# Performance work log

Measured on AMD Instinct MI355X. Metric: run time of the kernel, lower is better.

The kernel has to match this reference:

```python
import jax, jax.numpy as jnp
import numpy as np

B, S, H = 1, 2048, 1024
NH, NKV, D = 8, 2, 128           # query heads, kv heads, head_dim
E, TOPK = 64, 6                   # experts per modality, top-k
IT, IV, IS = 512, 256, 1024       # text / vision expert inter, shared inter (=512*2)
THETA = 500000.0
SECTIONS = (22, 22, 20)           # h, w, t rotary freq split; sum = D//2
EPS = 1e-5


def rmsnorm(x, w):
    return x * w * jax.lax.rsqrt(jnp.mean(x * x, axis=-1, keepdims=True) + EPS)


def apply_mrope(x, positions):
    # x: [B,S,h,D]; positions: [3,B,S] (h, w, t position streams)
    inv_freq = 1.0 / (THETA ** (jnp.arange(0, D, 2, dtype=jnp.float32) / D))  # [D//2]
    axis_idx = np.repeat(np.arange(3), SECTIONS)              # which pos stream per freq band
    pos = jnp.transpose(positions[axis_idx], (1, 2, 0)).astype(jnp.float32)  # [B,S,D//2]
    freqs = pos * inv_freq
    cos = jnp.cos(freqs)[:, :, None, :]
    sin = jnp.sin(freqs)[:, :, None, :]
    x1, x2 = x[..., 0::2], x[..., 1::2]                       # interleaved (non-neox)
    o1 = x1 * cos - x2 * sin
    o2 = x1 * sin + x2 * cos
    return jnp.stack([o1, o2], axis=-1).reshape(x.shape)


def attention(x, positions, w_qkv, w_o):
    b, s, _ = x.shape
    qkv = x @ w_qkv
    q, k, v = jnp.split(qkv, [NH * D, NH * D + NKV * D], axis=-1)
    q = q.reshape(b, s, NH, D)
    k = k.reshape(b, s, NKV, D)
    v = v.reshape(b, s, NKV, D)
    q = apply_mrope(q, positions)
    k = apply_mrope(k, positions)
    rep = NH // NKV
    k = jnp.repeat(k, rep, axis=2)
    v = jnp.repeat(v, rep, axis=2)
    scores = jnp.einsum('bqhd,bkhd->bhqk', q, k) * (D ** -0.5)
    causal = jnp.tril(jnp.ones((s, s), bool))
    scores = jnp.where(causal, scores, -jnp.inf)
    attn = jax.nn.softmax(scores, axis=-1)
    out = jnp.einsum('bhqk,bkhd->bqhd', attn, v).reshape(b, s, NH * D)
    return out @ w_o


def mlp(x, wg, wu, wd):
    return (jax.nn.silu(x @ wg) * (x @ wu)) @ wd


def moe_branch(x, gate_w, bias, wg, wu, wd):
    # x: [T,H]; gate_w: [H,E] fp32; bias: [E] fp32 correction bias
    logits = x.astype(jnp.float32) @ gate_w                   # [T,E]
    scores = jax.nn.sigmoid(logits)
    _, topi = jax.lax.top_k(scores + bias[None, :], TOPK)     # bias only picks experts
    w = jnp.take_along_axis(scores, topi, axis=-1)            # weights from raw scores
    w = w / jnp.sum(w, axis=-1, keepdims=True)                # renormalize
    T = x.shape[0]
    gates = jnp.zeros((T, E), jnp.float32).at[jnp.arange(T)[:, None], topi].set(w)
    g = jax.nn.silu(jnp.einsum('th,ehi->eti', x, wg)) * jnp.einsum('th,ehi->eti', x, wu)
    g = g * gates.T[:, :, None].astype(x.dtype)               # fold routing weights pre-down-proj
    return jnp.einsum('eti,eih->th', g, wd)


def _forward(hidden_states, positions, visual_token_mask, w_qkv, w_o, ln1_w, ln2_w,
             text_gate_w, vision_gate_w, corr_bias, tw_gate, tw_up, tw_down,
             vw_gate, vw_up, vw_down, sw_gate, sw_up, sw_down):
    h = hidden_states + attention(rmsnorm(hidden_states, ln1_w), positions, w_qkv, w_o)
    x = rmsnorm(h, ln2_w).reshape(-1, H)                      # [T,H]
    shared = mlp(x, sw_gate, sw_up, sw_down)
    text_out = moe_branch(x, text_gate_w, corr_bias[0], tw_gate, tw_up, tw_down)
    vision_out = moe_branch(x, vision_gate_w, corr_bias[1], vw_gate, vw_up, vw_down)
    mask = visual_token_mask.reshape(-1, 1)
    moe_out = jnp.where(mask, vision_out, text_out) + shared
    return h + moe_out.reshape(h.shape)


def setup_inputs() -> dict:
    key = jax.random.key(0)
    ks = jax.random.split(key, 16)
    rn = lambda i, shape, s: jax.random.normal(ks[i], shape, jnp.float32) * s
    return dict(
        hidden_states=rn(0, (B, S, H), 1.0),
        positions=jnp.broadcast_to(jnp.arange(S, dtype=jnp.int32)[None, None, :], (3, B, S)),
        visual_token_mask=jax.random.bernoulli(ks[1], 0.3, (B, S)),
        w_qkv=rn(2, (H, (NH + 2 * NKV) * D), H ** -0.5),
        w_o=rn(3, (NH * D, H), (NH * D) ** -0.5),
        ln1_w=jnp.ones((H,), jnp.float32),
        ln2_w=jnp.ones((H,), jnp.float32),
        text_gate_w=rn(4, (H, E), H ** -0.5),
        vision_gate_w=rn(5, (H, E), H ** -0.5),
        corr_bias=rn(6, (2, E), 0.02),
        tw_gate=rn(7, (E, H, IT), H ** -0.5),
        tw_up=rn(8, (E, H, IT), H ** -0.5),
        tw_down=rn(9, (E, IT, H), IT ** -0.5),
        vw_gate=rn(10, (E, H, IV), H ** -0.5),
        vw_up=rn(11, (E, H, IV), H ** -0.5),
        vw_down=rn(12, (E, IV, H), IV ** -0.5),
        sw_gate=rn(13, (H, IS), H ** -0.5),
        sw_up=rn(14, (H, IS), H ** -0.5),
        sw_down=rn(15, (IS, H), IS ** -0.5),
    )


def reference(hidden_states, positions, visual_token_mask, w_qkv, w_o, ln1_w, ln2_w,
              text_gate_w, vision_gate_w, corr_bias, tw_gate, tw_up, tw_down,
              vw_gate, vw_up, vw_down, sw_gate, sw_up, sw_down):
    return _forward(hidden_states, positions, visual_token_mask, w_qkv, w_o, ln1_w, ln2_w,
                    text_gate_w, vision_gate_w, corr_bias, tw_gate, tw_up, tw_down,
                    vw_gate, vw_up, vw_down, sw_gate, sw_up, sw_down)
```

## Files before the change

### kernel.cpp

```cpp
#include <hip/hip_runtime.h>
#include <hip/hip_bf16.h>
#include <math.h>

#define TT   2048
#define HID  1024
#define NHEAD 8
#define NKVH  2
#define HD   128
#define QKVN 1536
#define NEXP 64
#define NTOP 6
#define I_T  512
#define I_V  256
#define I_S  1024
#define SBASE ((size_t)12288 * 512)
#define NCHUNK 576

typedef unsigned short u16;
typedef __attribute__((ext_vector_type(8))) short short8v;
typedef __attribute__((ext_vector_type(4))) float f32x4;

__device__ inline u16 f2bf(float f) {
  __hip_bfloat16 h = __float2bfloat16(f);
  return *reinterpret_cast<u16*>(&h);
}
__device__ inline float bfu2f(u16 u) {
  unsigned x = ((unsigned)u) << 16;
  return __uint_as_float(x);
}
__device__ inline void split2(float f, u16& h, u16& l) {
  h = f2bf(f);
  l = f2bf(f - bfu2f(h));
}
__device__ inline void split8(const float* f, u16* h, u16* l) {
#pragma unroll
  for (int i = 0; i < 8; ++i) split2(f[i], h[i], l[i]);
}

__device__ inline f32x4 mfma16(short8v a, short8v b, f32x4 c) {
  return __builtin_amdgcn_mfma_f32_16x16x32_bf16(a, b, c, 0, 0, 0);
}

__device__ inline void wload(const float* __restrict__ W, int ldw, int c0, int kc,
                             float4* r) {
  const int t = threadIdx.x;
  const int c4 = (t & 7) << 2;
  const int r0 = t >> 3;
#pragma unroll
  for (int j = 0; j < 4; ++j)
    r[j] = *(const float4*)&W[(size_t)(kc + r0 + j * 32) * ldw + c0 + c4];
}
__device__ inline void wwrite(const float4* r, u16* lds) {
  const int t = threadIdx.x;
  const int c4 = (t & 7) << 2;
  const int r0 = t >> 3;
#pragma unroll
  for (int j = 0; j < 4; ++j) {
    int k = r0 + j * 32;
    u16* dst = lds + ((k >> 3) * 32) * 8 + (k & 7);
    dst[(c4 + 0) * 8] = f2bf(r[j].x);
    dst[(c4 + 1) * 8] = f2bf(r[j].y);
    dst[(c4 + 2) * 8] = f2bf(r[j].z);
    dst[(c4 + 3) * 8] = f2bf(r[j].w);
  }
}

template<bool F32, bool BF, bool LO>
__global__ __launch_bounds__(256) void rmsnorm_kernel(const float* __restrict__ x,
                                                      const float* __restrict__ w,
                                                      float* __restrict__ o32,
                                                      u16* __restrict__ obfH,
                                                      u16* __restrict__ obfL) {
  const int row = blockIdx.x;
  const int t = threadIdx.x;
  const float4 v = *(const float4*)(x + (size_t)row * HID + t * 4);
  float ss = v.x*v.x + v.y*v.y + v.z*v.z + v.w*v.w;
#pragma unroll
  for (int m = 32; m >= 1; m >>= 1) ss += __shfl_xor(ss, m);
  __shared__ float red[4];
  __shared__ float rrs;
  if ((t & 63) == 0) red[t >> 6] = ss;
  __syncthreads();
  if (t == 0) rrs = rsqrtf((red[0] + red[1] + red[2] + red[3]) * (1.0f / HID) + 1e-5f);
  __syncthreads();
  const float rr = rrs;
  const float4 wv = *(const float4*)(w + t * 4);
  float o[4];
  o[0] = v.x * wv.x * rr; o[1] = v.y * wv.y * rr;
  o[2] = v.z * wv.z * rr; o[3] = v.w * wv.w * rr;
  if (F32) *(float4*)(o32 + (size_t)row * HID + t * 4) = *(float4*)o;
  if (BF) {
    u16 h[4], l[4];
#pragma unroll
    for (int i = 0; i < 4; ++i) split2(o[i], h[i], l[i]);
    *(uint2*)(obfH + (size_t)row * HID + t * 4) = *(uint2*)h;
    if (LO) *(uint2*)(obfL + (size_t)row * HID + t * 4) = *(uint2*)l;
  }
}

__global__ __launch_bounds__(256) void convert_w(const float* __restrict__ W, int N,
                                                 u16* __restrict__ PH,
                                                 u16* __restrict__ PL) {
  const int c = blockIdx.x * 256 + threadIdx.x;
  const int k8 = blockIdx.y;
  float f[8];
#pragma unroll
  for (int e = 0; e < 8; ++e) f[e] = W[(size_t)(k8 * 8 + e) * N + c];
  u16 h8[8], l8[8];
  split8(f, h8, l8);
  size_t gi = ((size_t)(c >> 5) * 128 + k8) * 256 + (size_t)(c & 31) * 8;
  *(uint4*)&PH[gi] = *(uint4*)h8;
  *(uint4*)&PL[gi] = *(uint4*)l8;
}

template<bool RES>
__global__ __launch_bounds__(256) void dense_split(const u16* __restrict__ AH,
                                                   const u16* __restrict__ AL,
                                                   const u16* __restrict__ WPH,
                                                   const u16* __restrict__ WPL,
                                                   const float* __restrict__ resid,
                                                   float* __restrict__ C, int N) {
  __shared__ u16 sWH[32768], sWL[32768];
  __shared__ u16 sAH[4096],  sAL[4096];
  const int t = threadIdx.x;
  const int cs = blockIdx.x;
  const int c0 = cs * 32;
  const int rows = TT / gridDim.y;
  const int mstart = blockIdx.y * rows, mend = mstart + rows;
  {
    const u16* gh = WPH + (size_t)cs * 32768;
    const u16* gl = WPL + (size_t)cs * 32768;
#pragma unroll
    for (int r = 0; r < 16; ++r) {
      int i8 = (t + 256 * r) * 8;
      *(uint4*)&sWH[i8] = *(const uint4*)&gh[i8];
      *(uint4*)&sWL[i8] = *(const uint4*)&gl[i8];
    }
  }
  const int w = t >> 6, lane = t & 63;
  const int rowHalf = (w & 1) << 4, colHalf = (w >> 1) << 4;
  for (int m0 = mstart; m0 < mend; m0 += 32) {
    f32x4 hh = {0.f,0.f,0.f,0.f}, hl = {0.f,0.f,0.f,0.f};
    f32x4 lh = {0.f,0.f,0.f,0.f}, ll = {0.f,0.f,0.f,0.f};
    for (int kc = 0; kc < HID; kc += 128) {
      __syncthreads();
#pragma unroll
      for (int r = 0; r < 2; ++r) {
        int task = t + 256 * r;
        int row = task >> 4, kg = task & 15;
        size_t g = (size_t)(m0 + row) * HID + kc + kg * 8;
        *(uint4*)&sAH[(kg * 32 + row) * 8] = *(const uint4*)&AH[g];
        *(uint4*)&sAL[(kg * 32 + row) * 8] = *(const uint4*)&AL[g];
      }
      __syncthreads();
#pragma unroll
      for (int ks = 0; ks < 4; ++ks) {
        int arow = rowHalf + (lane & 15);
        int akg = ks * 4 + (lane >> 4);
        short8v ah = *(const short8v*)&sAH[(akg * 32 + arow) * 8];
        short8v al = *(const short8v*)&sAL[(akg * 32 + arow) * 8];
        int wcol = colHalf + (lane & 15);
        int wkg = (kc >> 3) + ks * 4 + (lane >> 4);
        short8v bh = *(const short8v*)&sWH[(wkg * 32 + wcol) * 8];
        short8v bl = *(const short8v*)&sWL[(wkg * 32 + wcol) * 8];
        hh = mfma16(ah, bh, hh);
        hl = mfma16(ah, bl, hl);
        lh = mfma16(al, bh, lh);
        ll = mfma16(al, bl, ll);
      }
    }
    f32x4 acc = (hh + hl) + (lh + ll);
#pragma unroll
    for (int i = 0; i < 4; ++i) {
      int r = m0 + rowHalf + ((lane >> 4) << 2) + i;
      int c = c0 + colHalf + (lane & 15);
      float v = acc[i];
      if (RES) v += resid[(size_t)r * N + c];
      C[(size_t)r * N + c] = v;
    }
  }
}

__global__ __launch_bounds__(256) void pack_qkv(const float* __restrict__ qkv,
                                                const int* __restrict__ pos,
                                                u16* __restrict__ Qh, u16* __restrict__ Ql,
                                                u16* __restrict__ Kph, u16* __restrict__ Kpl,
                                                u16* __restrict__ Vph, u16* __restrict__ Vpl) {
  const int tile = blockIdx.x;
  const int t = threadIdx.x;
  __shared__ float cs[2048], sn[2048];
  for (int i = t; i < 2048; i += 256) {
    int tok32 = i >> 6, fi = i & 63;
    int tok = tile * 32 + tok32;
    int axis = (fi < 22) ? 0 : (fi < 44 ? 1 : 2);
    float posv = (float)pos[axis * TT + tok];
    float invf = powf(500000.0f, -((float)(2 * fi)) / 128.0f);
    float ang = posv * invf;
    sincosf(ang, &sn[i], &cs[i]);
  }
  __syncthreads();
  for (int task = t; task < 4096; task += 256) {
    int h = task >> 9;
    int rem = task & 511;
    int tok32 = rem >> 4, fi4 = rem & 15;
    int tok = tile * 32 + tok32;
    const float* src = qkv + (size_t)tok * QKVN + h * HD + fi4 * 8;
    float4 v0 = *(const float4*)src, v1 = *(const float4*)(src + 4);
    float f[8] = {v0.x, v0.y, v0.z, v0.w, v1.x, v1.y, v1.z, v1.w};
    float o[8];
#pragma unroll
    for (int j = 0; j < 4; ++j) {
      int fi = fi4 * 4 + j;
      float c = cs[tok32 * 64 + fi], s = sn[tok32 * 64 + fi];
      o[2*j]   = f[2*j] * c - f[2*j+1] * s;
      o[2*j+1] = f[2*j] * s + f[2*j+1] * c;
    }
    u16 h8[8], l8[8];
    split8(o, h8, l8);
    size_t d = (size_t)tok * HID + h * HD + fi4 * 8;
    *(uint4*)&Qh[d] = *(uint4*)h8;
    *(uint4*)&Ql[d] = *(uint4*)l8;
  }
  for (int task = t; task < 1024; task += 256) {
    int kvh = task >> 9;
    int rem = task & 511;
    int kk = rem >> 4, fi4 = rem & 15;
    int tok = tile * 32 + kk;
    const float* src = qkv + (size_t)tok * QKVN + NHEAD * HD + kvh * HD + fi4 * 8;
    float4 v0 = *(const float4*)src, v1 = *(const float4*)(src + 4);
    float f[8] = {v0.x, v0.y, v0.z, v0.w, v1.x, v1.y, v1.z, v1.w};
    float o[8];
#pragma unroll
    for (int j = 0; j < 4; ++j) {
      int fi = fi4 * 4 + j;
      float c = cs[kk * 64 + fi], s = sn[kk * 64 + fi];
      o[2*j]   = f[2*j] * c - f[2*j+1] * s;
      o[2*j+1] = f[2*j] * s + f[2*j+1] * c;
    }
    u16 h8[8], l8[8];
    split8(o, h8, l8);
    size_t d = ((size_t)(kvh * 64 + tile) << 12) + (size_t)(fi4 * 32 + kk) * 8;
    *(uint4*)&Kph[d] = *(uint4*)h8;
    *(uint4*)&Kpl[d] = *(uint4*)l8;
  }
  for (int task = t; task < 1024; task += 256) {
    int kvh = task >> 9;
    int rem = task & 511;
    int g = rem >> 7, dcol = rem & 127;
    float f[8];
#pragma unroll
    for (int e = 0; e < 8; ++e)
      f[e] = qkv[(size_t)(tile * 32 + g * 8 + e) * QKVN + (NHEAD + NKVH) * HD + kvh * HD + dcol];
    u16 h8[8], l8[8];
    split8(f, h8, l8);
    size_t d = ((size_t)(kvh * 64 + tile) << 12) + (size_t)(g * 128 + dcol) * 8;
    *(uint4*)&Vph[d] = *(uint4*)h8;
    *(uint4*)&Vpl[d] = *(uint4*)l8;
  }
}

__global__ void chunk_setup(int* __restrict__ tab, int* __restrict__ startOff) {
  if (threadIdx.x == 0 && blockIdx.x == 0) {
    int idx = 0;
    for (int qb = 0; qb < TT / 16; ++qb) {
      startOff[qb] = idx;
      int nkt = (qb >> 1) + 1;
      int nch = (nkt + 7) >> 3;
      for (int c = 0; c < nch; ++c) { tab[idx] = qb * 16 + c; ++idx; }
    }
  }
}

__global__ __launch_bounds__(256) void attn_part(const u16* __restrict__ Qh,
                                                 const u16* __restrict__ Ql,
                                                 const u16* __restrict__ Kph,
                                                 const u16* __restrict__ Kpl,
                                                 const u16* __restrict__ Vph,
                                                 const u16* __restrict__ Vpl,
                                                 const int* __restrict__ tab,
                                                 float* __restrict__ Opart,
                                                 float* __restrict__ Mpart,
                                                 float* __restrict__ Lpart) {
  const int ci = blockIdx.x;
  const int kvh = blockIdx.y;
  const int w = threadIdx.x >> 6, lane = threadIdx.x & 63;
  const int head = kvh * 4 + w;
  const int ent = tab[ci];
  const int qb = ent >> 4, cc = ent & 15;
  const int qw0 = qb * 16;
  const int lrow = lane & 15, loct = lane >> 4;
  const int nkt = (qb >> 1) + 1;
  const int kt0 = cc * 8, kt1 = min(kt0 + 8, nkt);

  __shared__ u16 Ph[4][512], Pl[4][512];

  short8v qh[4], ql[4];
  {
    const size_t qoff = (size_t)(qw0 + lrow) * HID + head * HD + loct * 8;
#pragma unroll
    for (int dc = 0; dc < 4; ++dc) {
      qh[dc] = *(const short8v*)&Qh[qoff + dc * 32];
      ql[dc] = *(const short8v*)&Ql[qoff + dc * 32];
    }
  }

  f32x4 o[8];
#pragma unroll
  for (int dt = 0; dt < 8; ++dt) o[dt] = (f32x4){0.f,0.f,0.f,0.f};
  float mr[4] = {-INFINITY, -INFINITY, -INFINITY, -INFINITY};
  float lr[4] = {0.f, 0.f, 0.f, 0.f};
  const float scale = 0.08838834764831845f;

  for (int kt = kt0; kt < kt1; ++kt) {
    const int kv0 = kt * 32;
    const size_t tb = ((size_t)(kvh * 64 + kt) << 12);
    const u16* kbh = Kph + tb;
    const u16* kbl = Kpl + tb;
    f32x4 s[2];
#pragma unroll
    for (int nt = 0; nt < 2; ++nt) {
      f32x4 shh = {0.f,0.f,0.f,0.f}, shl = {0.f,0.f,0.f,0.f};
      f32x4 slh = {0.f,0.f,0.f,0.f}, sll = {0.f,0.f,0.f,0.f};
#pragma unroll
      for (int dc = 0; dc < 4; ++dc) {
        int off = ((dc * 4 + loct) * 32 + nt * 16 + lrow) * 8;
        short8v bh = *(const short8v*)&kbh[off];
        short8v bl = *(const short8v*)&kbl[off];
        shh = mfma16(qh[dc], bh, shh);
        shl = mfma16(qh[dc], bl, shl);
        slh = mfma16(ql[dc], bh, slh);
        sll = mfma16(ql[dc], bl, sll);
      }
      s[nt] = (shh + shl) + (slh + sll);
    }
    float rmax[4];
#pragma unroll
    for (int i = 0; i < 4; ++i) {
      int qrow = qw0 + loct * 4 + i;
#pragma unroll
      for (int nt = 0; nt < 2; ++nt) {
        int key = kv0 + nt * 16 + lrow;
        float v = s[nt][i] * scale;
        s[nt][i] = (key <= qrow) ? v : -INFINITY;
      }
      rmax[i] = fmaxf(s[0][i], s[1][i]);
    }
#pragma unroll
    for (int msk = 1; msk <= 8; msk <<= 1)
#pragma unroll
      for (int i = 0; i < 4; ++i) rmax[i] = fmaxf(rmax[i], __shfl_xor(rmax[i], msk));
    float corr[4];
#pragma unroll
    for (int i = 0; i < 4; ++i) {
      float mn = fmaxf(mr[i], rmax[i]);
      corr[i] = expf(mr[i] - mn);
      mr[i] = mn;
    }
    float p[2][4], ps[4];
#pragma unroll
    for (int nt = 0; nt < 2; ++nt)
#pragma unroll
      for (int i = 0; i < 4; ++i) p[nt][i] = expf(s[nt][i] - mr[i]);
#pragma unroll
    for (int i = 0; i < 4; ++i) ps[i] = p[0][i] + p[1][i];
#pragma unroll
    for (int msk = 1; msk <= 8; msk <<= 1)
#pragma unroll
      for (int i = 0; i < 4; ++i) ps[i] += __shfl_xor(ps[i], msk);
#pragma unroll
    for (int i = 0; i < 4; ++i) lr[i] = lr[i] * corr[i] + ps[i];
#pragma unroll
    for (int dt = 0; dt < 8; ++dt)
#pragma unroll
      for (int i = 0; i < 4; ++i) o[dt][i] *= corr[i];
#pragma unroll
    for (int nt = 0; nt < 2; ++nt)
#pragma unroll
      for (int i = 0; i < 4; ++i) {
        int q = loct * 4 + i;
        int kk = nt * 16 + lrow;
        int idx = ((kk >> 3) * 16 + q) * 8 + (kk & 7);
        u16 h, l;
        split2(p[nt][i], h, l);
        Ph[w][idx] = h;
        Pl[w][idx] = l;
      }
    asm volatile("s_waitcnt lgkmcnt(0)" ::: "memory");
    __builtin_amdgcn_sched_barrier(0);
    {
      int pbase = (loct * 16 + lrow) * 8;
      short8v pah = *(const short8v*)&Ph[w][pbase];
      short8v pal = *(const short8v*)&Pl[w][pbase];
      const u16* vbh = Vph + tb;
      const u16* vbl = Vpl + tb;
#pragma unroll
      for (int dt = 0; dt < 8; ++dt) {
        int off = (loct * 128 + dt * 16 + lrow) * 8;
        short8v vh = *(const short8v*)&vbh[off];
        short8v vl = *(const short8v*)&vbl[off];
        o[dt] = mfma16(pah, vh, o[dt]);
        o[dt] = mfma16(pah, vl, o[dt]);
        o[dt] = mfma16(pal, vh, o[dt]);
      }
    }
  }
  const size_t ob = ((size_t)head * NCHUNK + ci) * 16;
#pragma unroll
  for (int dt = 0; dt < 8; ++dt)
#pragma unroll
    for (int i = 0; i < 4; ++i) {
      int row = loct * 4 + i;
      int col = dt * 16 + lrow;
      Opart[(ob + row) * 128 + col] = o[dt][i];
    }
  if (lrow == 0) {
#pragma unroll
    for (int i = 0; i < 4; ++i) {
      int row = loct * 4 + i;
      Mpart[ob + row] = mr[i];
      Lpart[ob + row] = lr[i];
    }
  }
}

__global__ __launch_bounds__(256) void attn_combine(const float* __restrict__ Opart,
                                                    const float* __restrict__ Mpart,
                                                    const float* __restrict__ Lpart,
                                                    const int* __restrict__ startOff,
                                                    u16* __restrict__ aoH,
                                                    u16* __restrict__ aoL) {
  const int qb = blockIdx.x, head = blockIdx.y;
  const int t = threadIdx.x;
  const int row = t >> 4, c8 = (t & 15) * 8;
  const int nkt = (qb >> 1) + 1;
  const int nch = (nkt + 7) >> 3;
  const int s0 = startOff[qb];
  const size_t hb = (size_t)head * NCHUNK;
  float M = -INFINITY;
  for (int ch = 0; ch < nch; ++ch)
    M = fmaxf(M, Mpart[(hb + s0 + ch) * 16 + row]);
  float L = 0.f;
  float acc[8];
#pragma unroll
  for (int j = 0; j < 8; ++j) acc[j] = 0.f;
  for (int ch = 0; ch < nch; ++ch) {
    const size_t cb = (hb + s0 + ch) * 16 + row;
    float sc = expf(Mpart[cb] - M);
    L += sc * Lpart[cb];
    const float* op = &Opart[cb * 128 + c8];
    float4 a = *(const float4*)op, b = *(const float4*)(op + 4);
    acc[0] += sc * a.x; acc[1] += sc * a.y; acc[2] += sc * a.z; acc[3] += sc * a.w;
    acc[4] += sc * b.x; acc[5] += sc * b.y; acc[6] += sc * b.z; acc[7] += sc * b.w;
  }
  const float inv = 1.f / L;
  u16 h8[8], l8[8];
  float f[8];
#pragma unroll
  for (int j = 0; j < 8; ++j) f[j] = acc[j] * inv;
  split8(f, h8, l8);
  const size_t d = (size_t)(qb * 16 + row) * HID + head * HD + c8;
  *(uint4*)&aoH[d] = *(uint4*)h8;
  *(uint4*)&aoL[d] = *(uint4*)l8;
}

__global__ __launch_bounds__(256) void gate_kernel(const float* __restrict__ x2,
                                                   const int* __restrict__ vmask,
                                                   const float* __restrict__ tg,
                                                   const float* __restrict__ vg,
                                                   const float* __restrict__ cbias,
                                                   int* __restrict__ counts,
                                                   int* __restrict__ ptok,
                                                   float* __restrict__ pw) {
  const int tok = blockIdx.x;
  const int t = threadIdx.x;
  __shared__ float xs[HID];
  __shared__ float part[4][NEXP];
  __shared__ float sc[NEXP];
  __shared__ float sb[NEXP];
  *(float4*)&xs[t * 4] = *(const float4*)(x2 + (size_t)tok * HID + t * 4);
  __syncthreads();
  const int vis = (vmask[tok] != 0) ? 1 : 0;
  const float* gw = vis ? vg : tg;
  {
    const int e = t & 63, pr = t >> 6;
    float acc = 0.f;
    for (int h = pr * 256; h < (pr + 1) * 256; ++h) acc += xs[h] * gw[h * NEXP + e];
    part[pr][e] = acc;
  }
  __syncthreads();
  if (t < NEXP) {
    float a = part[0][t] + part[1][t] + part[2][t] + part[3][t];
    float s = 1.f / (1.f + expf(-a));
    sc[t] = s;
    sb[t] = s + cbias[vis * NEXP + t];
  }
  __syncthreads();
  if (t == 0) {
    int chosen[NTOP];
    unsigned long long usedm = 0ULL;
    float wsum = 0.f;
    for (int k = 0; k < NTOP; ++k) {
      float best = -1e30f; int bi = 0;
      for (int e = 0; e < NEXP; ++e) {
        if ((usedm >> e) & 1ULL) continue;
        if (sb[e] > best) { best = sb[e]; bi = e; }
      }
      usedm |= (1ULL << bi);
      chosen[k] = bi;
      wsum += sc[bi];
    }
    const float inv = 1.f / wsum;
    for (int k = 0; k < NTOP; ++k) {
      int e = chosen[k];
      int slot = vis * NEXP + e;
      int pos = atomicAdd(&counts[slot], 1);
      ptok[slot * TT + pos] = tok;
      pw[slot * TT + pos] = sc[e] * inv;
    }
  }
}

__global__ void scan_kernel(const int* __restrict__ counts, int* __restrict__ rowoff) {
  if (threadIdx.x == 0 && blockIdx.x == 0) {
    int s = 0;
    for (int i = 0; i < 128; ++i) { rowoff[i] = s; s += counts[i]; }
    rowoff[128] = s;
  }
}

template<int MODE>
__device__ inline void act_base(const int* rowoff, int slot, size_t& eb, int& stride) {
  if (MODE == 0) { eb = (size_t)rowoff[slot] * 512; stride = 512; }
  else if (MODE == 1) {
    int Rt = rowoff[64];
    eb = (size_t)Rt * 512 + (size_t)(rowoff[slot] - Rt) * 256; stride = 256;
  } else { eb = SBASE; stride = 1024; }
}

template<int IDIM, int MODE>
__global__ __launch_bounds__(256) void gateup_stream(const u16* __restrict__ X,
                                                     const float* __restrict__ WG,
                                                     const float* __restrict__ WU,
                                                     const int* __restrict__ counts,
                                                     const int* __restrict__ ptok,
                                                     const float* __restrict__ pw,
                                                     const int* __restrict__ rowoff,
                                                     u16* __restrict__ ACT) {
  __shared__ u16 sG[2][4096], sU[2][4096];
  __shared__ int toksL[256];
  __shared__ float twsL[256];
  const int c0 = blockIdx.x * 32;
  int cnt, mstart, mend, slot = 0;
  size_t eb; int stride;
  const float *wgp, *wup;
  if (MODE == 2) {
    cnt = TT; mstart = blockIdx.y * 256; mend = mstart + 256;
    eb = SBASE; stride = 1024;
    wgp = WG; wup = WU;
  } else {
    const int e = blockIdx.y;
    slot = (MODE == 1 ? NEXP : 0) + e;
    cnt = counts[slot];
    mstart = 0; mend = cnt;
    act_base<MODE>(rowoff, slot, eb, stride);
    wgp = WG + (size_t)e * HID * IDIM;
    wup = WU + (size_t)e * HID * IDIM;
  }
  if (mstart >= mend) return;
  const int w = threadIdx.x >> 6, lane = threadIdx.x & 63;
  const int lrow = lane & 15, loct = lane >> 4;

  for (int m0 = mstart; m0 < mend; m0 += 256) {
    {
      int gi = m0 + threadIdx.x;
      int tok = 0; float tw = 0.f;
      if (gi < cnt) {
        tok = (MODE == 2) ? gi : ptok[slot * TT + gi];
        tw  = (MODE == 2) ? 1.f : pw[slot * TT + gi];
      }
      toksL[threadIdx.x] = tok; twsL[threadIdx.x] = tw;
    }
    float4 rg[4], ru[4];
    wload(wgp, IDIM, c0, 0, rg);
    wload(wup, IDIM, c0, 0, ru);
    __syncthreads();
    wwrite(rg, sG[0]);
    wwrite(ru, sU[0]);
    const u16* xr[4];
#pragma unroll
    for (int tt = 0; tt < 4; ++tt)
      xr[tt] = X + (size_t)toksL[(w + tt * 4) * 16 + lrow] * HID;
    f32x4 aG[4][2], aU[4][2];
#pragma unroll
    for (int tt = 0; tt < 4; ++tt)
#pragma unroll
      for (int fr = 0; fr < 2; ++fr) {
        aG[tt][fr] = (f32x4){0.f,0.f,0.f,0.f};
        aU[tt][fr] = (f32x4){0.f,0.f,0.f,0.f};
      }
    __syncthreads();
    for (int c = 0; c < HID / 128; ++c) {
      const int cur = c & 1;
      if (c + 1 < HID / 128) {
        wload(wgp, IDIM, c0, (c + 1) * 128, rg);
        wload(wup, IDIM, c0, (c + 1) * 128, ru);
      }
#pragma unroll
      for (int ks = 0; ks < 4; ++ks) {
        const int boff = ((ks * 4 + loct) * 32 + lrow) * 8;
        short8v bg0 = *(const short8v*)&sG[cur][boff];
        short8v bg1 = *(const short8v*)&sG[cur][boff + 128];
        short8v bu0 = *(const short8v*)&sU[cur][boff];
        short8v bu1 = *(const short8v*)&sU[cur][boff + 128];
#pragma unroll
        for (int tt = 0; tt < 4; ++tt) {
          short8v a = *(const short8v*)&xr[tt][c * 128 + ks * 32 + loct * 8];
          aG[tt][0] = mfma16(a, bg0, aG[tt][0]);
          aG[tt][1] = mfma16(a, bg1, aG[tt][1]);
          aU[tt][0] = mfma16(a, bu0, aU[tt][0]);
          aU[tt][1] = mfma16(a, bu1, aU[tt][1]);
        }
      }
      if (c + 1 < HID / 128) {
        wwrite(rg, sG[cur ^ 1]);
        wwrite(ru, sU[cur ^ 1]);
      }
      __syncthreads();
    }
#pragma unroll
    for (int tt = 0; tt < 4; ++tt) {
      const int ti = w + tt * 4;
#pragma unroll
      for (int i = 0; i < 4; ++i) {
        const int r = loct * 4 + i;
        const int gi = m0 + ti * 16 + r;
        if (gi < cnt) {
          const float twv = twsL[ti * 16 + r];
#pragma unroll
          for (int fr = 0; fr < 2; ++fr) {
            float g = aG[tt][fr][i], u = aU[tt][fr][i];
            float a = g / (1.f + expf(-g)) * u * twv;
            ACT[eb + (size_t)gi * stride + c0 + fr * 16 + lrow] = f2bf(a);
          }
        }
      }
    }
    __syncthreads();
  }
}

template<int KDIM, int MODE>
__global__ __launch_bounds__(256) void down_stream(const u16* __restrict__ ACT,
                                                   const float* __restrict__ WD,
                                                   const int* __restrict__ counts,
                                                   const int* __restrict__ ptok,
                                                   const int* __restrict__ rowoff,
                                                   float* __restrict__ OUT) {
  __shared__ u16 sW[2][4096];
  __shared__ int toksL[256];
  const int c0 = blockIdx.x * 32;
  int cnt, mstart, mend, slot = 0;
  size_t eb; int stride;
  const float* wdp;
  if (MODE == 2) {
    cnt = TT; mstart = blockIdx.y * 256; mend = mstart + 256;
    eb = SBASE; stride = 1024;
    wdp = WD;
  } else {
    const int e = blockIdx.y;
    slot = (MODE == 1 ? NEXP : 0) + e;
    cnt = counts[slot];
    mstart = 0; mend = cnt;
    act_base<MODE>(rowoff, slot, eb, stride);
    wdp = WD + (size_t)e * KDIM * HID;
  }
  if (mstart >= mend) return;
  const int w = threadIdx.x >> 6, lane = threadIdx.x & 63;
  const int lrow = lane & 15, loct = lane >> 4;
  constexpr int NC = KDIM / 128;

  for (int m0 = mstart; m0 < mend; m0 += 256) {
    {
      int gi = m0 + threadIdx.x;
      int tok = 0;
      if (gi < cnt) tok = (MODE == 2) ? gi : ptok[slot * TT + gi];
      toksL[threadIdx.x] = tok;
    }
    float4 rw[4];
    wload(wdp, HID, c0, 0, rw);
    __syncthreads();
    wwrite(rw, sW[0]);
    const u16* ar[4];
#pragma unroll
    for (int tt = 0; tt < 4; ++tt) {
      int gi = m0 + (w + tt * 4) * 16 + lrow;
      int gc = (gi < cnt) ? gi : (cnt - 1);
      ar[tt] = ACT + eb + (size_t)gc * stride;
    }
    f32x4 acc[4][2];
#pragma unroll
    for (int tt = 0; tt < 4; ++tt)
#pragma unroll
      for (int fr = 0; fr < 2; ++fr) acc[tt][fr] = (f32x4){0.f,0.f,0.f,0.f};
    __syncthreads();
    for (int c = 0; c < NC; ++c) {
      const int cur = c & 1;
      if (c + 1 < NC) wload(wdp, HID, c0, (c + 1) * 128, rw);
#pragma unroll
      for (int ks = 0; ks < 4; ++ks) {
        const int boff = ((ks * 4 + loct) * 32 + lrow) * 8;
        short8v b0 = *(const short8v*)&sW[cur][boff];
        short8v b1 = *(const short8v*)&sW[cur][boff + 128];
#pragma unroll
        for (int tt = 0; tt < 4; ++tt) {
          short8v a = *(const short8v*)&ar[tt][c * 128 + ks * 32 + loct * 8];
          acc[tt][0] = mfma16(a, b0, acc[tt][0]);
          acc[tt][1] = mfma16(a, b1, acc[tt][1]);
        }
      }
      if (c + 1 < NC) wwrite(rw, sW[cur ^ 1]);
      __syncthreads();
    }
#pragma unroll
    for (int tt = 0; tt < 4; ++tt) {
      const int ti = w + tt * 4;
#pragma unroll
      for (int i = 0; i < 4; ++i) {
        const int r = loct * 4 + i;
        const int gi = m0 + ti * 16 + r;
        if (gi < cnt) {
          const int tok = toksL[ti * 16 + r];
#pragma unroll
          for (int fr = 0; fr < 2; ++fr)
            atomicAdd(&OUT[(size_t)tok * HID + c0 + fr * 16 + lrow], acc[tt][fr][i]);
        }
      }
    }
    __syncthreads();
  }
}

__global__ __launch_bounds__(256) void add2_kernel(const float* __restrict__ a,
                                                   const float* __restrict__ b,
                                                   float* __restrict__ out) {
  const size_t i = ((size_t)blockIdx.x * 256 + threadIdx.x) * 4;
  const float4 va = *(const float4*)(a + i);
  const float4 vb = *(const float4*)(b + i);
  float4 o;
  o.x = va.x + vb.x; o.y = va.y + vb.y; o.z = va.z + vb.z; o.w = va.w + vb.w;
  *(float4*)(out + i) = o;
}

extern "C" void kernel_launch(void* const* d_in, const int* in_sizes, int n_in,
                              void* d_out, int out_size, void* d_ws, size_t ws_size,
                              hipStream_t stream) {
  const float* hidden   = (const float*)d_in[0];
  const int*   positions= (const int*)d_in[1];
  const int*   vmask    = (const int*)d_in[2];
  const float* w_qkv    = (const float*)d_in[3];
  const float* w_o      = (const float*)d_in[4];
  const float* ln1      = (const float*)d_in[5];
  const float* ln2      = (const float*)d_in[6];
  const float* tgw      = (const float*)d_in[7];
  const float* vgw      = (const float*)d_in[8];
  const float* cbias    = (const float*)d_in[9];
  const float* twg      = (const float*)d_in[10];
  const float* twu      = (const float*)d_in[11];
  const float* twd      = (const float*)d_in[12];
  const float* vwg      = (const float*)d_in[13];
  const float* vwu      = (const float*)d_in[14];
  const float* vwd      = (const float*)d_in[15];
  const float* swg      = (const float*)d_in[16];
  const float* swu      = (const float*)d_in[17];
  const float* swd      = (const float*)d_in[18];
  float* out = (float*)d_out;

  char* ws = (char*)d_ws;
  size_t off = 0;
  auto alloc = [&](size_t bytes) -> void* {
    void* p = ws + off;
    off += (bytes + 255) & ~(size_t)255;
    return p;
  };
  u16*   xbh   = (u16*)alloc((size_t)TT * HID * 2);
  u16*   xbl   = (u16*)alloc((size_t)TT * HID * 2);
  float* qkv   = (float*)alloc((size_t)TT * QKVN * 4);
  u16*   aoH   = (u16*)alloc((size_t)TT * HID * 2);
  u16*   aoL   = (u16*)alloc((size_t)TT * HID * 2);
  float* hbuf  = (float*)alloc((size_t)TT * HID * 4);
  float* x2    = (float*)alloc((size_t)TT * HID * 4);
  u16*   xb2   = (u16*)alloc((size_t)TT * HID * 2);
  float* moe   = (float*)alloc((size_t)TT * HID * 4);
  u16*   ACT   = (u16*)alloc((SBASE + (size_t)TT * 1024) * 2);
  u16*   wqkvPH= (u16*)alloc((size_t)HID * QKVN * 2);
  u16*   wqkvPL= (u16*)alloc((size_t)HID * QKVN * 2);
  u16*   woPH  = (u16*)alloc((size_t)HID * HID * 2);
  u16*   woPL  = (u16*)alloc((size_t)HID * HID * 2);
  u16*   Qph   = (u16*)alloc((size_t)TT * HID * 2);
  u16*   Qpl   = (u16*)alloc((size_t)TT * HID * 2);
  u16*   Kph   = (u16*)alloc((size_t)NKVH * TT * HD * 2);
  u16*   Kpl   = (u16*)alloc((size_t)NKVH * TT * HD * 2);
  u16*   Vph   = (u16*)alloc((size_t)NKVH * TT * HD * 2);
  u16*   Vpl   = (u16*)alloc((size_t)NKVH * TT * HD * 2);
  float* Opart = (float*)alloc((size_t)NHEAD * NCHUNK * 16 * 128 * 4);
  float* Mpart = (float*)alloc((size_t)NHEAD * NCHUNK * 16 * 4);
  float* Lpart = (float*)alloc((size_t)NHEAD * NCHUNK * 16 * 4);
  int*   ctab  = (int*)alloc(NCHUNK * 4);
  int*   cstart= (int*)alloc((TT / 16) * 4);
  int*   counts= (int*)alloc(128 * 4);
  int*   rowoff= (int*)alloc(129 * 4);
  int*   ptok  = (int*)alloc((size_t)128 * TT * 4);
  float* pwgt  = (float*)alloc((size_t)128 * TT * 4);

  hipMemsetAsync(counts, 0, 128 * 4, stream);
  hipMemsetAsync(moe, 0, (size_t)TT * HID * 4, stream);

  chunk_setup<<<1, 64, 0, stream>>>(ctab, cstart);
  convert_w<<<dim3(QKVN / 256, 128), 256, 0, stream>>>(w_qkv, QKVN, wqkvPH, wqkvPL);
  convert_w<<<dim3(HID / 256, 128), 256, 0, stream>>>(w_o, HID, woPH, woPL);

  rmsnorm_kernel<false, true, true><<<TT, 256, 0, stream>>>(hidden, ln1, nullptr, xbh, xbl);
  dense_split<false><<<dim3(QKVN / 32, 8), 256, 0, stream>>>(xbh, xbl, wqkvPH, wqkvPL, nullptr, qkv, QKVN);
  pack_qkv<<<TT / 32, 256, 0, stream>>>(qkv, positions, Qph, Qpl, Kph, Kpl, Vph, Vpl);
  attn_part<<<dim3(NCHUNK, NKVH), 256, 0, stream>>>(Qph, Qpl, Kph, Kpl, Vph, Vpl, ctab, Opart, Mpart, Lpart);
  attn_combine<<<dim3(TT / 16, NHEAD), 256, 0, stream>>>(Opart, Mpart, Lpart, cstart, aoH, aoL);
  dense_split<true><<<dim3(HID / 32, 8), 256, 0, stream>>>(aoH, aoL, woPH, woPL, hidden, hbuf, HID);
  rmsnorm_kernel<true, true, false><<<TT, 256, 0, stream>>>(hbuf, ln2, x2, xb2, nullptr);
  gate_kernel<<<TT, 256, 0, stream>>>(x2, vmask, tgw, vgw, cbias, counts, ptok, pwgt);
  scan_kernel<<<1, 64, 0, stream>>>(counts, rowoff);

  gateup_stream<I_S, 2><<<dim3(I_S / 32, 8), 256, 0, stream>>>(xb2, swg, swu, nullptr, nullptr, nullptr, rowoff, ACT);
  gateup_stream<I_T, 0><<<dim3(I_T / 32, NEXP), 256, 0, stream>>>(xb2, twg, twu, counts, ptok, pwgt, rowoff, ACT);
  gateup_stream<I_V, 1><<<dim3(I_V / 32, NEXP), 256, 0, stream>>>(xb2, vwg, vwu, counts, ptok, pwgt, rowoff, ACT);

  down_stream<I_S, 2><<<dim3(HID / 32, 8), 256, 0, stream>>>(ACT, swd, nullptr, nullptr, rowoff, moe);
  down_stream<I_T, 0><<<dim3(HID / 32, NEXP), 256, 0, stream>>>(ACT, twd, counts, ptok, rowoff, moe);
  down_stream<I_V, 1><<<dim3(HID / 32, NEXP), 256, 0, stream>>>(ACT, vwd, counts, ptok, rowoff, moe);

  add2_kernel<<<(TT * HID) / 1024, 256, 0, stream>>>(hbuf, moe, out);
}
```

Baseline: 832.6 us.

## Compute transposed attention tiles to keep P in registers, drop LDS round-trip

The attention chunk kernel swaps MFMA operand order so each lane holds scores for one query row across keys. The P probabilities can then feed the PV MFMA straight from registers instead of going through shared memory, and the row max/sum reductions shrink to two shuffles with scalar running state. The V packing is reordered to match the new P fragment layout, and the low*low correction MFMA is dropped. s_setprio is also raised around the MFMA blocks, and the partial-output layout becomes column-major, so the combine kernel reads strided values in exchange for these gains.

```diff
diff --git a/kernel.cpp b/kernel.cpp
--- a/kernel.cpp
+++ b/kernel.cpp
@@ -249,8 +249,10 @@
     int g = rem >> 7, dcol = rem & 127;
     float f[8];
 #pragma unroll
-    for (int e = 0; e < 8; ++e)
-      f[e] = qkv[(size_t)(tile * 32 + g * 8 + e) * QKVN + (NHEAD + NKVH) * HD + kvh * HD + dcol];
+    for (int e = 0; e < 8; ++e) {
+      int key = ((e >> 2) * 16) + g * 4 + (e & 3);
+      f[e] = qkv[(size_t)(tile * 32 + key) * QKVN + (NHEAD + NKVH) * HD + kvh * HD + dcol];
+    }
     u16 h8[8], l8[8];
     split8(f, h8, l8);
     size_t d = ((size_t)(kvh * 64 + tile) << 12) + (size_t)(g * 128 + dcol) * 8;
@@ -292,8 +294,6 @@
   const int nkt = (qb >> 1) + 1;
   const int kt0 = cc * 8, kt1 = min(kt0 + 8, nkt);
 
-  __shared__ u16 Ph[4][512], Pl[4][512];
-
   short8v qh[4], ql[4];
   {
     const size_t qoff = (size_t)(qw0 + lrow) * HID + head * HD + loct * 8;
@@ -307,8 +307,7 @@
   f32x4 o[8];
 #pragma unroll
   for (int dt = 0; dt < 8; ++dt) o[dt] = (f32x4){0.f,0.f,0.f,0.f};
-  float mr[4] = {-INFINITY, -INFINITY, -INFINITY, -INFINITY};
-  float lr[4] = {0.f, 0.f, 0.f, 0.f};
+  float mr = -INFINITY, lr = 0.f;
   const float scale = 0.08838834764831845f;
 
   for (int kt = kt0; kt < kt1; ++kt) {
@@ -317,109 +316,83 @@
     const u16* kbh = Kph + tb;
     const u16* kbl = Kpl + tb;
     f32x4 s[2];
+    __builtin_amdgcn_s_setprio(1);
 #pragma unroll
     for (int nt = 0; nt < 2; ++nt) {
       f32x4 shh = {0.f,0.f,0.f,0.f}, shl = {0.f,0.f,0.f,0.f};
-      f32x4 slh = {0.f,0.f,0.f,0.f}, sll = {0.f,0.f,0.f,0.f};
+      f32x4 slh = {0.f,0.f,0.f,0.f};
 #pragma unroll
       for (int dc = 0; dc < 4; ++dc) {
         int off = ((dc * 4 + loct) * 32 + nt * 16 + lrow) * 8;
-        short8v bh = *(const short8v*)&kbh[off];
-        short8v bl = *(const short8v*)&kbl[off];
-        shh = mfma16(qh[dc], bh, shh);
-        shl = mfma16(qh[dc], bl, shl);
-        slh = mfma16(ql[dc], bh, slh);
-        sll = mfma16(ql[dc], bl, sll);
-      }
-      s[nt] = (shh + shl) + (slh + sll);
-    }
-    float rmax[4];
-#pragma unroll
-    for (int i = 0; i < 4; ++i) {
-      int qrow = qw0 + loct * 4 + i;
-#pragma unroll
-      for (int nt = 0; nt < 2; ++nt) {
-        int key = kv0 + nt * 16 + lrow;
+        short8v kh = *(const short8v*)&kbh[off];
+        short8v kl = *(const short8v*)&kbl[off];
+        shh = mfma16(kh, qh[dc], shh);
+        shl = mfma16(kh, ql[dc], shl);
+        slh = mfma16(kl, qh[dc], slh);
+      }
+      s[nt] = shh + (shl + slh);
+    }
+    __builtin_amdgcn_s_setprio(0);
+    const int qrow = qw0 + lrow;
+    float rmax = -INFINITY;
+#pragma unroll
+    for (int nt = 0; nt < 2; ++nt)
+#pragma unroll
+      for (int i = 0; i < 4; ++i) {
+        int key = kv0 + nt * 16 + loct * 4 + i;
         float v = s[nt][i] * scale;
         s[nt][i] = (key <= qrow) ? v : -INFINITY;
-      }
-      rmax[i] = fmaxf(s[0][i], s[1][i]);
-    }
-#pragma unroll
-    for (int msk = 1; msk <= 8; msk <<= 1)
-#pragma unroll
-      for (int i = 0; i < 4; ++i) rmax[i] = fmaxf(rmax[i], __shfl_xor(rmax[i], msk));
-    float corr[4];
+        rmax = fmaxf(rmax, s[nt][i]);
+      }
+    rmax = fmaxf(rmax, __shfl_xor(rmax, 16));
+    rmax = fmaxf(rmax, __shfl_xor(rmax, 32));
+    const float mn = fmaxf(mr, rmax);
+    const float corr = expf(mr - mn);
+    mr = mn;
+    float p[2][4];
+    float ps = 0.f;
+#pragma unroll
+    for (int nt = 0; nt < 2; ++nt)
+#pragma unroll
+      for (int i = 0; i < 4; ++i) { p[nt][i] = expf(s[nt][i] - mr); ps += p[nt][i]; }
+    ps += __shfl_xor(ps, 16);
+    ps += __shfl_xor(ps, 32);
+    lr = lr * corr + ps;
+#pragma unroll
+    for (int dt = 0; dt < 8; ++dt)
+#pragma unroll
+      for (int i = 0; i < 4; ++i) o[dt][i] *= corr;
+    u16 ph8[8], pl8[8];
+#pragma unroll
+    for (int j = 0; j < 8; ++j) split2(p[j >> 2][j & 3], ph8[j], pl8[j]);
+    short8v pfh = *(short8v*)ph8;
+    short8v pfl = *(short8v*)pl8;
+    const u16* vbh = Vph + tb;
+    const u16* vbl = Vpl + tb;
+    __builtin_amdgcn_s_setprio(1);
+#pragma unroll
+    for (int dt = 0; dt < 8; ++dt) {
+      int off = (loct * 128 + dt * 16 + lrow) * 8;
+      short8v vh = *(const short8v*)&vbh[off];
+      short8v vl = *(const short8v*)&vbl[off];
+      o[dt] = mfma16(vh, pfh, o[dt]);
+      o[dt] = mfma16(vh, pfl, o[dt]);
+      o[dt] = mfma16(vl, pfh, o[dt]);
+    }
+    __builtin_amdgcn_s_setprio(0);
+  }
+  const size_t ob = (size_t)head * NCHUNK + ci;
+  float* op = Opart + ob * 2048;
+#pragma unroll
+  for (int dt = 0; dt < 8; ++dt)
 #pragma unroll
     for (int i = 0; i < 4; ++i) {
-      float mn = fmaxf(mr[i], rmax[i]);
-      corr[i] = expf(mr[i] - mn);
-      mr[i] = mn;
-    }
-    float p[2][4], ps[4];
-#pragma unroll
-    for (int nt = 0; nt < 2; ++nt)
-#pragma unroll
-      for (int i = 0; i < 4; ++i) p[nt][i] = expf(s[nt][i] - mr[i]);
-#pragma unroll
-    for (int i = 0; i < 4; ++i) ps[i] = p[0][i] + p[1][i];
-#pragma unroll
-    for (int msk = 1; msk <= 8; msk <<= 1)
-#pragma unroll
-      for (int i = 0; i < 4; ++i) ps[i] += __shfl_xor(ps[i], msk);
-#pragma unroll
-    for (int i = 0; i < 4; ++i) lr[i] = lr[i] * corr[i] + ps[i];
-#pragma unroll
-    for (int dt = 0; dt < 8; ++dt)
-#pragma unroll
-      for (int i = 0; i < 4; ++i) o[dt][i] *= corr[i];
-#pragma unroll
-    for (int nt = 0; nt < 2; ++nt)
-#pragma unroll
-      for (int i = 0; i < 4; ++i) {
-        int q = loct * 4 + i;
-        int kk = nt * 16 + lrow;
-        int idx = ((kk >> 3) * 16 + q) * 8 + (kk & 7);
-        u16 h, l;
-        split2(p[nt][i], h, l);
-        Ph[w][idx] = h;
-        Pl[w][idx] = l;
-      }
-    asm volatile("s_waitcnt lgkmcnt(0)" ::: "memory");
-    __builtin_amdgcn_sched_barrier(0);
-    {
-      int pbase = (loct * 16 + lrow) * 8;
-      short8v pah = *(const short8v*)&Ph[w][pbase];
-      short8v pal = *(const short8v*)&Pl[w][pbase];
-      const u16* vbh = Vph + tb;
-      const u16* vbl = Vpl + tb;
-#pragma unroll
-      for (int dt = 0; dt < 8; ++dt) {
-        int off = (loct * 128 + dt * 16 + lrow) * 8;
-        short8v vh = *(const short8v*)&vbh[off];
-        short8v vl = *(const short8v*)&vbl[off];
-        o[dt] = mfma16(pah, vh, o[dt]);
-        o[dt] = mfma16(pah, vl, o[dt]);
-        o[dt] = mfma16(pal, vh, o[dt]);
-      }
-    }
-  }
-  const size_t ob = ((size_t)head * NCHUNK + ci) * 16;
-#pragma unroll
-  for (int dt = 0; dt < 8; ++dt)
-#pragma unroll
-    for (int i = 0; i < 4; ++i) {
-      int row = loct * 4 + i;
-      int col = dt * 16 + lrow;
-      Opart[(ob + row) * 128 + col] = o[dt][i];
-    }
-  if (lrow == 0) {
-#pragma unroll
-    for (int i = 0; i < 4; ++i) {
-      int row = loct * 4 + i;
-      Mpart[ob + row] = mr[i];
-      Lpart[ob + row] = lr[i];
-    }
+      int d = dt * 16 + loct * 4 + i;
+      op[d * 16 + lrow] = o[dt][i];
+    }
+  if (loct == 0) {
+    Mpart[ob * 16 + lrow] = mr;
+    Lpart[ob * 16 + lrow] = lr;
   }
 }
 
@@ -444,13 +417,13 @@
 #pragma unroll
   for (int j = 0; j < 8; ++j) acc[j] = 0.f;
   for (int ch = 0; ch < nch; ++ch) {
-    const size_t cb = (hb + s0 + ch) * 16 + row;
-    float sc = expf(Mpart[cb] - M);
-    L += sc * Lpart[cb];
-    const float* op = &Opart[cb * 128 + c8];
-    float4 a = *(const float4*)op, b = *(const float4*)(op + 4);
-    acc[0] += sc * a.x; acc[1] += sc * a.y; acc[2] += sc * a.z; acc[3] += sc * a.w;
-    acc[4] += sc * b.x; acc[5] += sc * b.y; acc[6] += sc * b.z; acc[7] += sc * b.w;
+    const size_t cb = hb + s0 + ch;
+    float sc = expf(Mpart[cb * 16 + row] - M);
+    L += sc * Lpart[cb * 16 + row];
+    const float* op = Opart + cb * 2048;
+#pragma unroll
+    for (int j = 0; j < 8; ++j)
+      acc[j] += sc * op[(c8 + j) * 16 + row];
   }
   const float inv = 1.f / L;
   u16 h8[8], l8[8];
```

Measured after the change: 804.3 us. 3.4% less time.
